# Optimization experiments

Measured on AMD Instinct MI355X. Metric: run time of the kernel, lower is better.

## Reference

```python
import jax, jax.numpy as jnp
import numpy as np

B, S, E_BERT = 64, 512, 768
H = 64        # GRU hidden per direction (hidden_dim=128 bidirectional)
T = 16        # num output tags
P = 32        # pos_num_tags = attention embed dim


def setup_inputs() -> dict:
    key = jax.random.key(0)
    ks = jax.random.split(key, 20)
    def n(k, shape, s=0.1):
        return jax.random.normal(k, shape, dtype=jnp.float32) * s
    return {
        "bert_embed": n(ks[0], (B, S, E_BERT), 1.0),
        "input2": n(ks[1], (B, S, P), 1.0),
        "targets": jax.random.randint(ks[2], (B, S), 0, T),
        # forward-direction GRU (torch layout: W_ih (3H,E), W_hh (3H,H))
        "Wih_f": n(ks[3], (3 * H, E_BERT)), "Whh_f": n(ks[4], (3 * H, H)),
        "bih_f": n(ks[5], (3 * H,)), "bhh_f": n(ks[6], (3 * H,)),
        # backward-direction GRU
        "Wih_b": n(ks[7], (3 * H, E_BERT)), "Whh_b": n(ks[8], (3 * H, H)),
        "bih_b": n(ks[9], (3 * H,)), "bhh_b": n(ks[10], (3 * H,)),
        # dense (no bias): (2H -> T)
        "Wdense": n(ks[11], (2 * H, T)),
        # single-head MultiheadAttention over pos features
        "in_proj_w": n(ks[12], (3 * P, P)), "in_proj_b": n(ks[13], (3 * P,)),
        "out_proj_w": n(ks[14], (P, P)), "out_proj_b": n(ks[15], (P,)),
        # fusion linear (no bias): (T+P -> T)
        "Wfuse": n(ks[16], (T + P, T)),
        # CRF params
        "crf_start": n(ks[17], (T,)), "crf_end": n(ks[18], (T,)),
        "crf_trans": n(ks[19], (T, T)),
    }


def _gru_dir(x, Wih, Whh, bih, bhh, reverse):
    # x: (B,S,E) -> outputs (B,S,H); torch GRU cell math.
    xp = jnp.einsum('bse,ge->bsg', x, Wih) + bih      # precompute input gates (B,S,3H)
    xp = jnp.swapaxes(xp, 0, 1)                        # (S,B,3H)
    h0 = jnp.zeros((x.shape[0], Whh.shape[1]), x.dtype)
    def step(h, xt):
        gh = h @ Whh.T + bhh
        xr, xz, xn = jnp.split(xt, 3, axis=-1)
        hr, hz, hn = jnp.split(gh, 3, axis=-1)
        r = jax.nn.sigmoid(xr + hr)
        z = jax.nn.sigmoid(xz + hz)
        nw = jnp.tanh(xn + r * hn)
        h = (1.0 - z) * nw + z * h
        return h, h
    _, ys = jax.lax.scan(step, h0, xp, reverse=reverse)
    return jnp.swapaxes(ys, 0, 1)                      # (B,S,H)


def _forward(bert_embed, input2, targets,
             Wih_f, Whh_f, bih_f, bhh_f,
             Wih_b, Whh_b, bih_b, bhh_b,
             Wdense, in_proj_w, in_proj_b, out_proj_w, out_proj_b,
             Wfuse, crf_start, crf_end, crf_trans):
    # Bi-GRU over frozen BERT embeddings
    fwd = _gru_dir(bert_embed, Wih_f, Whh_f, bih_f, bhh_f, False)
    bwd = _gru_dir(bert_embed, Wih_b, Whh_b, bih_b, bhh_b, True)
    lstm_out = jnp.concatenate([fwd, bwd], axis=-1)    # (B,S,2H)
    dense = lstm_out @ Wdense                          # (B,S,T)

    # single-head self-attention on POS features (torch MultiheadAttention)
    qkv = input2 @ in_proj_w.T + in_proj_b
    q, k, v = jnp.split(qkv, 3, axis=-1)
    scores = jnp.einsum('bqd,bkd->bqk', q, k) / jnp.sqrt(jnp.float32(P))
    attn = jnp.einsum('bqk,bkd->bqd', jax.nn.softmax(scores, axis=-1), v)
    attn = attn @ out_proj_w.T + out_proj_b            # (B,S,P)

    # fusion -> emissions
    emis = jnp.concatenate([dense, attn], axis=-1) @ Wfuse  # (B,S,T)

    # CRF NLL (torchcrf, full mask, reduction='mean')
    em_tags = jnp.take_along_axis(emis, targets[..., None], axis=2)[..., 0]  # (B,S)
    numerator = (crf_start[targets[:, 0]]
                 + em_tags.sum(axis=-1)
                 + crf_trans[targets[:, :-1], targets[:, 1:]].sum(axis=-1)
                 + crf_end[targets[:, -1]])

    def step(score, em_t):  # score (B,T), em_t (B,T)
        nxt = jax.nn.logsumexp(score[:, :, None] + crf_trans[None] + em_t[:, None, :], axis=1)
        return nxt, None
    score0 = crf_start[None] + emis[:, 0]
    scoreF, _ = jax.lax.scan(step, score0, jnp.swapaxes(emis[:, 1:], 0, 1))
    denominator = jax.nn.logsumexp(scoreF + crf_end[None], axis=1)

    return jnp.mean(denominator - numerator)  # -mean(log_likelihood)


def reference(bert_embed, input2, targets,
              Wih_f, Whh_f, bih_f, bhh_f,
              Wih_b, Whh_b, bih_b, bhh_b,
              Wdense, in_proj_w, in_proj_b, out_proj_w, out_proj_b,
              Wfuse, crf_start, crf_end, crf_trans):
    return _forward(bert_embed, input2, targets,
                    Wih_f, Whh_f, bih_f, bhh_f,
                    Wih_b, Whh_b, bih_b, bhh_b,
                    Wdense, in_proj_w, in_proj_b, out_proj_w, out_proj_b,
                    Wfuse, crf_start, crf_end, crf_trans)
```

## Files before the change

kernel.cpp:

```cpp
#include <hip/hip_runtime.h>

#define Bn 64
#define Sn 512
#define EB 768
#define Hn 64
#define G3 192
#define Tn 16
#define Pn 32

__device__ __forceinline__ float sigmoidf_(float x) { return 1.f / (1.f + __expf(-x)); }
__device__ __forceinline__ float tanhf_(float x) { return 1.f - 2.f / (__expf(2.f * x) + 1.f); }

__device__ __forceinline__ unsigned short f2bf(float x) {
  union { float f; unsigned u; } v; v.f = x;
  unsigned r = v.u + 0x7fff + ((v.u >> 16) & 1);
  return (unsigned short)(r >> 16);
}

typedef __attribute__((ext_vector_type(8))) short short8;
typedef __attribute__((ext_vector_type(4))) float f32x4;

__global__ __launch_bounds__(256) void mega_a(const float* __restrict__ A,
                                              const float* __restrict__ Wf,
                                              const float* __restrict__ Wb,
                                              const float* __restrict__ bf,
                                              const float* __restrict__ bb,
                                              float* __restrict__ C,
                                              const float* __restrict__ in2,
                                              const float* __restrict__ Wqkv,
                                              const float* __restrict__ bqkv,
                                              float* __restrict__ qb,
                                              float* __restrict__ kb,
                                              float* __restrict__ vb,
                                              const float* __restrict__ Wdense,
                                              const float* __restrict__ Wfuse,
                                              float* __restrict__ wcomb) {
  __shared__ __align__(16) char smem[20864];
  const int gblk = blockIdx.x;
  const int tid = threadIdx.x;
  if (gblk < 768) {
    unsigned short* As = (unsigned short*)smem;
    unsigned short* Bs = As + 128 * 40;
    const int g = gblk;
    const int xcd = g & 7;
    const int slot = g >> 3;
    const int lin = xcd * 96 + slot;
    const int m_tile = lin / 3;
    const int n_tile = lin % 3;
    const int n0 = n_tile * 128;
    const int m0 = m_tile * 128;
    const int wv = tid >> 6;
    const int lane = tid & 63;
    const int wm = (wv >> 1) * 64, wn = (wv & 1) * 64;
    const int fr = lane & 15, fq = lane >> 4;
    const int srow = tid >> 1;
    const int shalf = (tid & 1) * 16;
    const int bcol = n0 + srow;
    const float* Wrow = (bcol < G3) ? (Wf + (size_t)bcol * EB) : (Wb + (size_t)(bcol - G3) * EB);
    const float* Arow = A + (size_t)(m0 + srow) * EB;
    f32x4 acc[4][4];
#pragma unroll
    for (int i = 0; i < 4; ++i)
#pragma unroll
      for (int j = 0; j < 4; ++j) acc[i][j] = (f32x4){0.f, 0.f, 0.f, 0.f};
    for (int k0 = 0; k0 < EB; k0 += 32) {
      float4 a0 = *(const float4*)&Arow[k0 + shalf + 0];
      float4 a1 = *(const float4*)&Arow[k0 + shalf + 4];
      float4 a2 = *(const float4*)&Arow[k0 + shalf + 8];
      float4 a3 = *(const float4*)&Arow[k0 + shalf + 12];
      float4 b0 = *(const float4*)&Wrow[k0 + shalf + 0];
      float4 b1 = *(const float4*)&Wrow[k0 + shalf + 4];
      float4 b2 = *(const float4*)&Wrow[k0 + shalf + 8];
      float4 b3 = *(const float4*)&Wrow[k0 + shalf + 12];
      __syncthreads();
      short8 pa, pb;
      pa[0] = f2bf(a0.x); pa[1] = f2bf(a0.y); pa[2] = f2bf(a0.z); pa[3] = f2bf(a0.w);
      pa[4] = f2bf(a1.x); pa[5] = f2bf(a1.y); pa[6] = f2bf(a1.z); pa[7] = f2bf(a1.w);
      *(short8*)&As[srow * 40 + shalf] = pa;
      pa[0] = f2bf(a2.x); pa[1] = f2bf(a2.y); pa[2] = f2bf(a2.z); pa[3] = f2bf(a2.w);
      pa[4] = f2bf(a3.x); pa[5] = f2bf(a3.y); pa[6] = f2bf(a3.z); pa[7] = f2bf(a3.w);
      *(short8*)&As[srow * 40 + shalf + 8] = pa;
      pb[0] = f2bf(b0.x); pb[1] = f2bf(b0.y); pb[2] = f2bf(b0.z); pb[3] = f2bf(b0.w);
      pb[4] = f2bf(b1.x); pb[5] = f2bf(b1.y); pb[6] = f2bf(b1.z); pb[7] = f2bf(b1.w);
      *(short8*)&Bs[srow * 40 + shalf] = pb;
      pb[0] = f2bf(b2.x); pb[1] = f2bf(b2.y); pb[2] = f2bf(b2.z); pb[3] = f2bf(b2.w);
      pb[4] = f2bf(b3.x); pb[5] = f2bf(b3.y); pb[6] = f2bf(b3.z); pb[7] = f2bf(b3.w);
      *(short8*)&Bs[srow * 40 + shalf + 8] = pb;
      __syncthreads();
      short8 af[4], bfv[4];
#pragma unroll
      for (int i = 0; i < 4; ++i) af[i] = *(short8*)&As[(wm + i * 16 + fr) * 40 + fq * 8];
#pragma unroll
      for (int j = 0; j < 4; ++j) bfv[j] = *(short8*)&Bs[(wn + j * 16 + fr) * 40 + fq * 8];
#pragma unroll
      for (int i = 0; i < 4; ++i)
#pragma unroll
        for (int j = 0; j < 4; ++j)
          acc[i][j] = __builtin_amdgcn_mfma_f32_16x16x32_bf16(af[i], bfv[j], acc[i][j], 0, 0, 0);
    }
#pragma unroll
    for (int j = 0; j < 4; ++j) {
      int col = n0 + wn + j * 16 + fr;
      float bias = (col < G3) ? bf[col] : bb[col - G3];
#pragma unroll
      for (int i = 0; i < 4; ++i) {
        int rowb = m0 + wm + i * 16 + fq * 4;
#pragma unroll
        for (int rg = 0; rg < 4; ++rg)
          C[(size_t)(rowb + rg) * 384 + col] = acc[i][j][rg] + bias;
      }
    }
  } else if (gblk < 896) {
    float* Ws = (float*)smem;
    float* bs = Ws + 96 * 32;
    for (int i = tid; i < 96 * 32; i += 256) Ws[i] = Wqkv[i];
    if (tid < 96) bs[tid] = bqkv[tid];
    __syncthreads();
    const int idx = (gblk - 768) * 256 + tid;
    float x[32];
#pragma unroll
    for (int d4 = 0; d4 < 8; ++d4) {
      float4 v = *(const float4*)&in2[(size_t)idx * 32 + d4 * 4];
      x[d4 * 4 + 0] = v.x; x[d4 * 4 + 1] = v.y; x[d4 * 4 + 2] = v.z; x[d4 * 4 + 3] = v.w;
    }
    float* const dsts[3] = {qb, kb, vb};
#pragma unroll
    for (int p = 0; p < 3; ++p) {
      float a[32];
#pragma unroll
      for (int j = 0; j < 32; ++j) {
        float s = bs[p * 32 + j];
#pragma unroll
        for (int d = 0; d < 32; ++d) s += x[d] * Ws[(p * 32 + j) * 32 + d];
        a[j] = s;
      }
      float* dst = dsts[p];
#pragma unroll
      for (int j4 = 0; j4 < 8; ++j4) {
        float4 o = {a[j4 * 4 + 0], a[j4 * 4 + 1], a[j4 * 4 + 2], a[j4 * 4 + 3]};
        *(float4*)&dst[(size_t)idx * 32 + j4 * 4] = o;
      }
    }
  } else {
    int e = (gblk - 896) * 256 + tid;
    int i = e >> 4, j = e & 15;
    float a = 0.f;
#pragma unroll
    for (int c = 0; c < 16; ++c) a += Wdense[i * 16 + c] * Wfuse[c * 16 + j];
    wcomb[e] = a;
  }
}

__global__ __launch_bounds__(256, 1) void mega_b(const float* __restrict__ C,
                                                 const float* __restrict__ Whh_f,
                                                 const float* __restrict__ bhh_f,
                                                 const float* __restrict__ Whh_b,
                                                 const float* __restrict__ bhh_b,
                                                 float* __restrict__ out,
                                                 const float* __restrict__ qb,
                                                 const float* __restrict__ kb,
                                                 const float* __restrict__ vb,
                                                 float* __restrict__ part) {
  __shared__ __align__(16) char smem[33280];
  const int tid = threadIdx.x;
  if (blockIdx.x < 128) {
    float* xs = (float*)smem;
    float* hbuf = xs + 32 * 192;
    float* obuf = hbuf + 128;
    const int wg = blockIdx.x;
    const int rev = (wg >= Bn) ? 1 : 0;
    const int b = wg & (Bn - 1);
    const int w = tid >> 6;
    const int lane = tid & 63;
    const int r = lane >> 2;
    const int kc = lane & 3;
    const int row = 16 * w + r;
    const int k0 = 16 * kc;
    const float* Whh = rev ? Whh_b : Whh_f;
    const float* bhh = rev ? bhh_b : bhh_f;
    const int colBase = rev ? G3 : 0;
    const int dirOff = rev ? Hn : 0;
    float4 wv[3][4];
#pragma unroll
    for (int g = 0; g < 3; ++g)
#pragma unroll
      for (int q = 0; q < 4; ++q) {
        wv[g][q] = *(const float4*)&Whh[(size_t)(g * 64 + row) * 64 + k0 + 4 * q];
        asm volatile("" : "+v"(wv[g][q].x), "+v"(wv[g][q].y), "+v"(wv[g][q].z), "+v"(wv[g][q].w));
      }
    const float brr = bhh[row], bzz = bhh[64 + row], bnn = bhh[128 + row];
    if (tid < 64) { hbuf[tid] = 0.f; hbuf[64 + tid] = 0.f; }
    float h = 0.f;
    for (int c = 0; c < 16; ++c) {
      const int cstart = c * 32;
      if (c > 0) {
#pragma unroll
        for (int i = 0; i < 2; ++i) {
          int f = tid + 256 * i;
          int s = f >> 4;
          int c4 = (f & 15) << 2;
          int tp = cstart - 32 + s;
          int orow = rev ? (Sn - 1 - tp) : tp;
          *(float4*)&out[(size_t)(b * Sn + orow) * 128 + dirOff + c4] = *(const float4*)&obuf[s * 64 + c4];
        }
      }
      float4 st[6];
#pragma unroll
      for (int i = 0; i < 6; ++i) {
        int f = tid + 256 * i;
        int s = f / 48;
        int c4 = (f % 48) << 2;
        int t = cstart + s;
        int grow = rev ? (Sn - 1 - t) : t;
        st[i] = *(const float4*)&C[(size_t)(b * Sn + grow) * 384 + colBase + c4];
      }
#pragma unroll
      for (int i = 0; i < 6; ++i) {
        int f = tid + 256 * i;
        int s = f / 48;
        int c4 = (f % 48) << 2;
        *(float4*)&xs[s * 192 + c4] = st[i];
      }
      __syncthreads();
      float xr = xs[row], xz = xs[64 + row], xn = xs[128 + row];
      for (int s = 0; s < 32; ++s) {
        const int t = cstart + s;
        const int p = t & 1;
        float4 ha = *(const float4*)&hbuf[p * 64 + k0 + 0];
        float4 hb = *(const float4*)&hbuf[p * 64 + k0 + 4];
        float4 hc = *(const float4*)&hbuf[p * 64 + k0 + 8];
        float4 hd = *(const float4*)&hbuf[p * 64 + k0 + 12];
        float nxr = 0.f, nxz = 0.f, nxn = 0.f;
        if (s + 1 < 32) {
          const float* xq = &xs[(s + 1) * 192];
          nxr = xq[row]; nxz = xq[64 + row]; nxn = xq[128 + row];
        }
        float dr, dz, dn;
        {
          float4 wa, wbv, wc, wd;
          wa = wv[0][0]; wbv = wv[0][1]; wc = wv[0][2]; wd = wv[0][3];
          dr = (wa.x * ha.x + wa.y * ha.y + wa.z * ha.z + wa.w * ha.w)
             + (wbv.x * hb.x + wbv.y * hb.y + wbv.z * hb.z + wbv.w * hb.w)
             + (wc.x * hc.x + wc.y * hc.y + wc.z * hc.z + wc.w * hc.w)
             + (wd.x * hd.x + wd.y * hd.y + wd.z * hd.z + wd.w * hd.w);
          wa = wv[1][0]; wbv = wv[1][1]; wc = wv[1][2]; wd = wv[1][3];
          dz = (wa.x * ha.x + wa.y * ha.y + wa.z * ha.z + wa.w * ha.w)
             + (wbv.x * hb.x + wbv.y * hb.y + wbv.z * hb.z + wbv.w * hb.w)
             + (wc.x * hc.x + wc.y * hc.y + wc.z * hc.z + wc.w * hc.w)
             + (wd.x * hd.x + wd.y * hd.y + wd.z * hd.z + wd.w * hd.w);
          wa = wv[2][0]; wbv = wv[2][1]; wc = wv[2][2]; wd = wv[2][3];
          dn = (wa.x * ha.x + wa.y * ha.y + wa.z * ha.z + wa.w * ha.w)
             + (wbv.x * hb.x + wbv.y * hb.y + wbv.z * hb.z + wbv.w * hb.w)
             + (wc.x * hc.x + wc.y * hc.y + wc.z * hc.z + wc.w * hc.w)
             + (wd.x * hd.x + wd.y * hd.y + wd.z * hd.z + wd.w * hd.w);
        }
        dr += __shfl_xor(dr, 1); dr += __shfl_xor(dr, 2);
        dz += __shfl_xor(dz, 1); dz += __shfl_xor(dz, 2);
        dn += __shfl_xor(dn, 1); dn += __shfl_xor(dn, 2);
        float rg = sigmoidf_(xr + brr + dr);
        float zg = sigmoidf_(xz + bzz + dz);
        float ng = tanhf_(xn + rg * (bnn + dn));
        h = (1.f - zg) * ng + zg * h;
        if (kc == 0) {
          hbuf[(p ^ 1) * 64 + row] = h;
          obuf[s * 64 + row] = h;
        }
        __syncthreads();
        xr = nxr; xz = nxz; xn = nxn;
      }
    }
#pragma unroll
    for (int i = 0; i < 2; ++i) {
      int f = tid + 256 * i;
      int s = f >> 4;
      int c4 = (f & 15) << 2;
      int tp = Sn - 32 + s;
      int orow = rev ? (Sn - 1 - tp) : tp;
      *(float4*)&out[(size_t)(b * Sn + orow) * 128 + dirOff + c4] = *(const float4*)&obuf[s * 64 + c4];
    }
  } else {
    float* Ks = (float*)smem;
    float* Vs = Ks + 128 * 32;
    const int blk = blockIdx.x - 128;
    const int b = blk >> 3;
    const int qhalf = (blk >> 2) & 1;
    const int split = blk & 3;
    const int k0 = split * 128;
#pragma unroll
    for (int i = 0; i < 4; ++i) {
      int f = tid + 256 * i;
      int row = f >> 3, col = (f & 7) * 4;
      *(float4*)&Ks[row * 32 + col] = *(const float4*)&kb[(size_t)(b * Sn + k0 + row) * 32 + col];
      *(float4*)&Vs[row * 32 + col] = *(const float4*)&vb[(size_t)(b * Sn + k0 + row) * 32 + col];
    }
    const int q = b * Sn + qhalf * 256 + tid;
    float qv[32];
#pragma unroll
    for (int d4 = 0; d4 < 8; ++d4) {
      float4 v = *(const float4*)&qb[(size_t)q * 32 + d4 * 4];
      qv[d4 * 4 + 0] = v.x; qv[d4 * 4 + 1] = v.y; qv[d4 * 4 + 2] = v.z; qv[d4 * 4 + 3] = v.w;
    }
    __syncthreads();
    const float scale = 0.17677669529663687f;
    float m = -1e30f, lsum = 0.f;
    float acc[32] = {};
    for (int kk = 0; kk < 128; ++kk) {
      const float4* kr = (const float4*)&Ks[kk * 32];
      float s = 0.f;
#pragma unroll
      for (int d4 = 0; d4 < 8; ++d4) {
        float4 kv = kr[d4];
        s += qv[d4 * 4 + 0] * kv.x + qv[d4 * 4 + 1] * kv.y + qv[d4 * 4 + 2] * kv.z + qv[d4 * 4 + 3] * kv.w;
      }
      s *= scale;
      float mn = fmaxf(m, s);
      float e1 = __expf(m - mn);
      float p = __expf(s - mn);
      lsum = lsum * e1 + p;
      const float4* vr = (const float4*)&Vs[kk * 32];
#pragma unroll
      for (int d4 = 0; d4 < 8; ++d4) {
        float4 vv = vr[d4];
        acc[d4 * 4 + 0] = acc[d4 * 4 + 0] * e1 + p * vv.x;
        acc[d4 * 4 + 1] = acc[d4 * 4 + 1] * e1 + p * vv.y;
        acc[d4 * 4 + 2] = acc[d4 * 4 + 2] * e1 + p * vv.z;
        acc[d4 * 4 + 3] = acc[d4 * 4 + 3] * e1 + p * vv.w;
      }
      m = mn;
    }
    float* rec = part + ((size_t)q * 4 + split) * 36;
#pragma unroll
    for (int d4 = 0; d4 < 8; ++d4) {
      float4 o = {acc[d4 * 4 + 0], acc[d4 * 4 + 1], acc[d4 * 4 + 2], acc[d4 * 4 + 3]};
      *(float4*)&rec[d4 * 4] = o;
    }
    rec[32] = m;
    rec[33] = lsum;
  }
}

__global__ __launch_bounds__(256) void attn_combine(const float* __restrict__ part,
                                                    const float* __restrict__ Wout,
                                                    const float* __restrict__ bout,
                                                    float* __restrict__ attn) {
  __shared__ float Ws[32 * 32];
  __shared__ float bs[32];
  const int tid = threadIdx.x;
  for (int i = tid; i < 1024; i += 256) Ws[i] = Wout[i];
  if (tid < 32) bs[tid] = bout[tid];
  __syncthreads();
  const int q = blockIdx.x * 256 + tid;
  const float* rec = part + (size_t)q * 4 * 36;
  float m0 = rec[32], m1 = rec[36 + 32], m2 = rec[72 + 32], m3 = rec[108 + 32];
  float M = fmaxf(fmaxf(m0, m1), fmaxf(m2, m3));
  float w0 = __expf(m0 - M), w1 = __expf(m1 - M), w2 = __expf(m2 - M), w3 = __expf(m3 - M);
  float L = rec[33] * w0 + rec[36 + 33] * w1 + rec[72 + 33] * w2 + rec[108 + 33] * w3;
  float inv = 1.f / L;
  float a[32];
#pragma unroll
  for (int d4 = 0; d4 < 8; ++d4) {
    float4 p0 = *(const float4*)&rec[d4 * 4];
    float4 p1 = *(const float4*)&rec[36 + d4 * 4];
    float4 p2 = *(const float4*)&rec[72 + d4 * 4];
    float4 p3 = *(const float4*)&rec[108 + d4 * 4];
    a[d4 * 4 + 0] = (p0.x * w0 + p1.x * w1 + p2.x * w2 + p3.x * w3) * inv;
    a[d4 * 4 + 1] = (p0.y * w0 + p1.y * w1 + p2.y * w2 + p3.y * w3) * inv;
    a[d4 * 4 + 2] = (p0.z * w0 + p1.z * w1 + p2.z * w2 + p3.z * w3) * inv;
    a[d4 * 4 + 3] = (p0.w * w0 + p1.w * w1 + p2.w * w2 + p3.w * w3) * inv;
  }
#pragma unroll
  for (int j = 0; j < 32; ++j) {
    float o = bs[j];
#pragma unroll
    for (int d = 0; d < 32; ++d) o += a[d] * Ws[j * 32 + d];
    attn[(size_t)q * 32 + j] = o;
  }
}

__global__ __launch_bounds__(256) void emis_kernel(const float* __restrict__ lstm,
                                                   const float* __restrict__ attn,
                                                   const float* __restrict__ wcomb,
                                                   const float* __restrict__ Wfuse,
                                                   float* __restrict__ emis) {
  __shared__ float Wc[128 * 16];
  __shared__ float Wf2[32 * 16];
  const int tid = threadIdx.x;
  for (int i = tid; i < 2048; i += 256) Wc[i] = wcomb[i];
  for (int i = tid; i < 512; i += 256) Wf2[i] = Wfuse[16 * 16 + i];
  __syncthreads();
  const int idx = blockIdx.x * 256 + tid;
  float acc[16] = {};
  for (int i = 0; i < 128; i += 4) {
    float4 lv = *(const float4*)&lstm[(size_t)idx * 128 + i];
    float ll[4] = {lv.x, lv.y, lv.z, lv.w};
#pragma unroll
    for (int u = 0; u < 4; ++u)
#pragma unroll
      for (int j = 0; j < 16; ++j) acc[j] += ll[u] * Wc[(i + u) * 16 + j];
  }
  for (int d = 0; d < 32; d += 4) {
    float4 av = *(const float4*)&attn[(size_t)idx * 32 + d];
    float aa[4] = {av.x, av.y, av.z, av.w};
#pragma unroll
    for (int u = 0; u < 4; ++u)
#pragma unroll
      for (int j = 0; j < 16; ++j) acc[j] += aa[u] * Wf2[(d + u) * 16 + j];
  }
#pragma unroll
  for (int j = 0; j < 16; j += 4) {
    float4 o = {acc[j], acc[j + 1], acc[j + 2], acc[j + 3]};
    *(float4*)&emis[(size_t)idx * 16 + j] = o;
  }
}

__global__ __launch_bounds__(64) void mega_e(const float* __restrict__ emis,
                                             const int* __restrict__ tgt,
                                             const float* __restrict__ cstart,
                                             const float* __restrict__ cend,
                                             const float* __restrict__ ctrans,
                                             float* __restrict__ numer,
                                             float* __restrict__ denom) {
  if (blockIdx.x < 64) {
    const int b = blockIdx.x, l = threadIdx.x;
    float ssum = 0.f;
    for (int t = l; t < Sn; t += 64) {
      int tg = tgt[b * Sn + t];
      ssum += emis[(size_t)(b * Sn + t) * Tn + tg];
      if (t + 1 < Sn) {
        int tg2 = tgt[b * Sn + t + 1];
        ssum += ctrans[tg * Tn + tg2];
      }
    }
    if (l == 0) ssum += cstart[tgt[b * Sn]] + cend[tgt[b * Sn + Sn - 1]];
    for (int off = 32; off > 0; off >>= 1) ssum += __shfl_down(ssum, off);
    if (l == 0) numer[b] = ssum;
  } else {
    const int b = blockIdx.x - 64;
    const int lane = threadIdx.x;
    const int g = lane >> 4;
    const int j = lane & 15;
    const int i0 = 4 * g;
    float tr0 = ctrans[(i0 + 0) * Tn + j];
    float tr1 = ctrans[(i0 + 1) * Tn + j];
    float tr2 = ctrans[(i0 + 2) * Tn + j];
    float tr3 = ctrans[(i0 + 3) * Tn + j];
    float s = cstart[j] + emis[(size_t)(b * Sn) * Tn + j];
    float em = emis[(size_t)(b * Sn + 1) * Tn + j];
    for (int t = 1; t < Sn; ++t) {
      float s0 = __shfl(s, i0 + 0);
      float s1 = __shfl(s, i0 + 1);
      float s2 = __shfl(s, i0 + 2);
      float s3 = __shfl(s, i0 + 3);
      float v0 = s0 + tr0, v1 = s1 + tr1, v2 = s2 + tr2, v3 = s3 + tr3;
      float m = fmaxf(fmaxf(v0, v1), fmaxf(v2, v3));
      m = fmaxf(m, __shfl_xor(m, 16));
      m = fmaxf(m, __shfl_xor(m, 32));
      float e = __expf(v0 - m) + __expf(v1 - m) + __expf(v2 - m) + __expf(v3 - m);
      e += __shfl_xor(e, 16);
      e += __shfl_xor(e, 32);
      float em_cur = em;
      if (t + 1 < Sn) em = emis[(size_t)(b * Sn + t + 1) * Tn + j];
      s = em_cur + m + __logf(e);
    }
    float f = s + cend[j];
    float m = f;
    m = fmaxf(m, __shfl_xor(m, 1));
    m = fmaxf(m, __shfl_xor(m, 2));
    m = fmaxf(m, __shfl_xor(m, 4));
    m = fmaxf(m, __shfl_xor(m, 8));
    float e = __expf(f - m);
    e += __shfl_xor(e, 1);
    e += __shfl_xor(e, 2);
    e += __shfl_xor(e, 4);
    e += __shfl_xor(e, 8);
    if (lane == 0) denom[b] = m + __logf(e);
  }
}

__global__ __launch_bounds__(64) void final_kernel(const float* __restrict__ numer,
                                                   const float* __restrict__ denom,
                                                   float* __restrict__ out) {
  const int l = threadIdx.x;
  float d = denom[l] - numer[l];
  for (int off = 32; off > 0; off >>= 1) d += __shfl_down(d, off);
  if (l == 0) out[0] = d * (1.f / 64.f);
}

extern "C" void kernel_launch(void* const* d_in, const int* in_sizes, int n_in,
                              void* d_out, int out_size, void* d_ws, size_t ws_size,
                              hipStream_t stream) {
  (void)in_sizes; (void)n_in; (void)out_size; (void)ws_size;
  const float* bert = (const float*)d_in[0];
  const float* in2 = (const float*)d_in[1];
  const int* tgt = (const int*)d_in[2];
  const float* Wih_f = (const float*)d_in[3];
  const float* Whh_f = (const float*)d_in[4];
  const float* bih_f = (const float*)d_in[5];
  const float* bhh_f = (const float*)d_in[6];
  const float* Wih_b = (const float*)d_in[7];
  const float* Whh_b = (const float*)d_in[8];
  const float* bih_b = (const float*)d_in[9];
  const float* bhh_b = (const float*)d_in[10];
  const float* Wdense = (const float*)d_in[11];
  const float* in_proj_w = (const float*)d_in[12];
  const float* in_proj_b = (const float*)d_in[13];
  const float* out_proj_w = (const float*)d_in[14];
  const float* out_proj_b = (const float*)d_in[15];
  const float* Wfuse = (const float*)d_in[16];
  const float* cstart = (const float*)d_in[17];
  const float* cend = (const float*)d_in[18];
  const float* ctrans = (const float*)d_in[19];

  float* ws = (float*)d_ws;
  float* C = ws;
  float* lstm = C + (size_t)Bn * Sn * 384;
  float* qb = lstm + (size_t)Bn * Sn * 2 * Hn;
  float* kb = qb + (size_t)Bn * Sn * Pn;
  float* vb = kb + (size_t)Bn * Sn * Pn;
  float* attn = vb + (size_t)Bn * Sn * Pn;
  float* emis = attn + (size_t)Bn * Sn * Pn;
  float* wcomb = emis + (size_t)Bn * Sn * Tn;
  float* numer = wcomb + 128 * 16;
  float* denom = numer + Bn;
  float* part = denom + Bn;

  mega_a<<<904, 256, 0, stream>>>(bert, Wih_f, Wih_b, bih_f, bih_b, C,
                                  in2, in_proj_w, in_proj_b, qb, kb, vb,
                                  Wdense, Wfuse, wcomb);
  mega_b<<<640, 256, 0, stream>>>(C, Whh_f, bhh_f, Whh_b, bhh_b, lstm,
                                  qb, kb, vb, part);
  attn_combine<<<Bn * Sn / 256, 256, 0, stream>>>(part, out_proj_w, out_proj_b, attn);
  emis_kernel<<<Bn * Sn / 256, 256, 0, stream>>>(lstm, attn, wcomb, Wfuse, emis);
  mega_e<<<128, 64, 0, stream>>>(emis, tgt, cstart, cend, ctrans, numer, denom);
  final_kernel<<<1, 64, 0, stream>>>(numer, denom, (float*)d_out);
}
```

Before: 621.1 us.

## Pre-convert GEMM operands to bf16 and use direct global-to-LDS loads; fuse attn combine with emission

Adds a separate pass that converts bert embeddings and input weights to bf16 in workspace. The input-projection GEMM then streams them into LDS with global_load_lds instead of loading fp32, converting in registers and storing to LDS. The attention-combine and emission kernels are merged so the attention output stays in registers and is never written to or reread from global memory. The conversion pass reads the full fp32 tensor and writes a bf16 copy, which adds traffic and a launch. The GEMM also drops LDS padding, which may cause bank conflicts, and its loop has no double buffering.

Measured after the change: 704.2 us. 1.13x slower.

```diff
diff --git a/kernel.cpp b/kernel.cpp
--- a/kernel.cpp
+++ b/kernel.cpp
@@ -20,9 +20,34 @@
 typedef __attribute__((ext_vector_type(8))) short short8;
 typedef __attribute__((ext_vector_type(4))) float f32x4;
 
-__global__ __launch_bounds__(256) void mega_a(const float* __restrict__ A,
-                                              const float* __restrict__ Wf,
-                                              const float* __restrict__ Wb,
+__device__ __forceinline__ void gload_lds16(const unsigned short* g, unsigned short* l) {
+  __builtin_amdgcn_global_load_lds((const __attribute__((address_space(1))) unsigned int*)g,
+                                   (__attribute__((address_space(3))) unsigned int*)l, 16, 0, 0);
+}
+
+__global__ __launch_bounds__(256) void convert_kernel(const float* __restrict__ bert,
+                                                      const float* __restrict__ Wf,
+                                                      const float* __restrict__ Wb,
+                                                      unsigned short* __restrict__ Abf,
+                                                      unsigned short* __restrict__ Wbf) {
+  const int blk = blockIdx.x;
+  const float* src;
+  unsigned short* dst;
+  size_t base;
+  if (blk < 12288) { src = bert; dst = Abf; base = (size_t)blk * 2048; }
+  else if (blk < 12360) { src = Wf; dst = Wbf; base = (size_t)(blk - 12288) * 2048; }
+  else { src = Wb; dst = Wbf + 147456; base = (size_t)(blk - 12360) * 2048; }
+  size_t e = base + (size_t)threadIdx.x * 8;
+  float4 v0 = *(const float4*)&src[e];
+  float4 v1 = *(const float4*)&src[e + 4];
+  short8 o;
+  o[0] = f2bf(v0.x); o[1] = f2bf(v0.y); o[2] = f2bf(v0.z); o[3] = f2bf(v0.w);
+  o[4] = f2bf(v1.x); o[5] = f2bf(v1.y); o[6] = f2bf(v1.z); o[7] = f2bf(v1.w);
+  *(short8*)&dst[e] = o;
+}
+
+__global__ __launch_bounds__(256) void mega_a(const unsigned short* __restrict__ Abf,
+                                              const unsigned short* __restrict__ Wbf,
                                               const float* __restrict__ bf,
                                               const float* __restrict__ bb,
                                               float* __restrict__ C,
@@ -35,15 +60,14 @@
                                               const float* __restrict__ Wdense,
                                               const float* __restrict__ Wfuse,
                                               float* __restrict__ wcomb) {
-  __shared__ __align__(16) char smem[20864];
+  __shared__ __align__(16) char smem[16384];
   const int gblk = blockIdx.x;
   const int tid = threadIdx.x;
   if (gblk < 768) {
     unsigned short* As = (unsigned short*)smem;
-    unsigned short* Bs = As + 128 * 40;
-    const int g = gblk;
-    const int xcd = g & 7;
-    const int slot = g >> 3;
+    unsigned short* Bs = As + 128 * 32;
+    const int xcd = gblk & 7;
+    const int slot = gblk >> 3;
     const int lin = xcd * 96 + slot;
     const int m_tile = lin / 3;
     const int n_tile = lin % 3;
@@ -53,50 +77,38 @@
     const int lane = tid & 63;
     const int wm = (wv >> 1) * 64, wn = (wv & 1) * 64;
     const int fr = lane & 15, fq = lane >> 4;
-    const int srow = tid >> 1;
-    const int shalf = (tid & 1) * 16;
-    const int bcol = n0 + srow;
-    const float* Wrow = (bcol < G3) ? (Wf + (size_t)bcol * EB) : (Wb + (size_t)(bcol - G3) * EB);
-    const float* Arow = A + (size_t)(m0 + srow) * EB;
+    const int c0 = (wv * 2 + 0) * 64 + lane;
+    const int c1 = (wv * 2 + 1) * 64 + lane;
+    const unsigned short* Asrc0 = Abf + (size_t)(m0 + (c0 >> 2)) * EB + (c0 & 3) * 8;
+    const unsigned short* Asrc1 = Abf + (size_t)(m0 + (c1 >> 2)) * EB + (c1 & 3) * 8;
+    const unsigned short* Bsrc0 = Wbf + (size_t)(n0 + (c0 >> 2)) * EB + (c0 & 3) * 8;
+    const unsigned short* Bsrc1 = Wbf + (size_t)(n0 + (c1 >> 2)) * EB + (c1 & 3) * 8;
+    unsigned short* Adst0 = As + (wv * 2 + 0) * 64 * 8;
+    unsigned short* Adst1 = As + (wv * 2 + 1) * 64 * 8;
+    unsigned short* Bdst0 = Bs + (wv * 2 + 0) * 64 * 8;
+    unsigned short* Bdst1 = Bs + (wv * 2 + 1) * 64 * 8;
     f32x4 acc[4][4];
 #pragma unroll
     for (int i = 0; i < 4; ++i)
 #pragma unroll
       for (int j = 0; j < 4; ++j) acc[i][j] = (f32x4){0.f, 0.f, 0.f, 0.f};
     for (int k0 = 0; k0 < EB; k0 += 32) {
-      float4 a0 = *(const float4*)&Arow[k0 + shalf + 0];
-      float4 a1 = *(const float4*)&Arow[k0 + shalf + 4];
-      float4 a2 = *(const float4*)&Arow[k0 + shalf + 8];
-      float4 a3 = *(const float4*)&Arow[k0 + shalf + 12];
-      float4 b0 = *(const float4*)&Wrow[k0 + shalf + 0];
-      float4 b1 = *(const float4*)&Wrow[k0 + shalf + 4];
-      float4 b2 = *(const float4*)&Wrow[k0 + shalf + 8];
-      float4 b3 = *(const float4*)&Wrow[k0 + shalf + 12];
-      __syncthreads();
-      short8 pa, pb;
-      pa[0] = f2bf(a0.x); pa[1] = f2bf(a0.y); pa[2] = f2bf(a0.z); pa[3] = f2bf(a0.w);
-      pa[4] = f2bf(a1.x); pa[5] = f2bf(a1.y); pa[6] = f2bf(a1.z); pa[7] = f2bf(a1.w);
-      *(short8*)&As[srow * 40 + shalf] = pa;
-      pa[0] = f2bf(a2.x); pa[1] = f2bf(a2.y); pa[2] = f2bf(a2.z); pa[3] = f2bf(a2.w);
-      pa[4] = f2bf(a3.x); pa[5] = f2bf(a3.y); pa[6] = f2bf(a3.z); pa[7] = f2bf(a3.w);
-      *(short8*)&As[srow * 40 + shalf + 8] = pa;
-      pb[0] = f2bf(b0.x); pb[1] = f2bf(b0.y); pb[2] = f2bf(b0.z); pb[3] = f2bf(b0.w);
-      pb[4] = f2bf(b1.x); pb[5] = f2bf(b1.y); pb[6] = f2bf(b1.z); pb[7] = f2bf(b1.w);
-      *(short8*)&Bs[srow * 40 + shalf] = pb;
-      pb[0] = f2bf(b2.x); pb[1] = f2bf(b2.y); pb[2] = f2bf(b2.z); pb[3] = f2bf(b2.w);
-      pb[4] = f2bf(b3.x); pb[5] = f2bf(b3.y); pb[6] = f2bf(b3.z); pb[7] = f2bf(b3.w);
-      *(short8*)&Bs[srow * 40 + shalf + 8] = pb;
+      gload_lds16(Asrc0 + k0, Adst0);
+      gload_lds16(Asrc1 + k0, Adst1);
+      gload_lds16(Bsrc0 + k0, Bdst0);
+      gload_lds16(Bsrc1 + k0, Bdst1);
       __syncthreads();
       short8 af[4], bfv[4];
 #pragma unroll
-      for (int i = 0; i < 4; ++i) af[i] = *(short8*)&As[(wm + i * 16 + fr) * 40 + fq * 8];
-#pragma unroll
-      for (int j = 0; j < 4; ++j) bfv[j] = *(short8*)&Bs[(wn + j * 16 + fr) * 40 + fq * 8];
+      for (int i = 0; i < 4; ++i) af[i] = *(short8*)&As[(wm + i * 16 + fr) * 32 + fq * 8];
+#pragma unroll
+      for (int j = 0; j < 4; ++j) bfv[j] = *(short8*)&Bs[(wn + j * 16 + fr) * 32 + fq * 8];
 #pragma unroll
       for (int i = 0; i < 4; ++i)
 #pragma unroll
         for (int j = 0; j < 4; ++j)
           acc[i][j] = __builtin_amdgcn_mfma_f32_16x16x32_bf16(af[i], bfv[j], acc[i][j], 0, 0, 0);
+      __syncthreads();
     }
 #pragma unroll
     for (int j = 0; j < 4; ++j) {
@@ -339,15 +351,22 @@
   }
 }
 
-__global__ __launch_bounds__(256) void attn_combine(const float* __restrict__ part,
-                                                    const float* __restrict__ Wout,
-                                                    const float* __restrict__ bout,
-                                                    float* __restrict__ attn) {
+__global__ __launch_bounds__(256) void comb_emis(const float* __restrict__ part,
+                                                 const float* __restrict__ Wout,
+                                                 const float* __restrict__ bout,
+                                                 const float* __restrict__ lstm,
+                                                 const float* __restrict__ wcomb,
+                                                 const float* __restrict__ Wfuse,
+                                                 float* __restrict__ emis) {
   __shared__ float Ws[32 * 32];
   __shared__ float bs[32];
+  __shared__ float Wc[128 * 16];
+  __shared__ float Wf2[32 * 16];
   const int tid = threadIdx.x;
   for (int i = tid; i < 1024; i += 256) Ws[i] = Wout[i];
   if (tid < 32) bs[tid] = bout[tid];
+  for (int i = tid; i < 2048; i += 256) Wc[i] = wcomb[i];
+  for (int i = tid; i < 512; i += 256) Wf2[i] = Wfuse[16 * 16 + i];
   __syncthreads();
   const int q = blockIdx.x * 256 + tid;
   const float* rec = part + (size_t)q * 4 * 36;
@@ -368,48 +387,31 @@
     a[d4 * 4 + 2] = (p0.z * w0 + p1.z * w1 + p2.z * w2 + p3.z * w3) * inv;
     a[d4 * 4 + 3] = (p0.w * w0 + p1.w * w1 + p2.w * w2 + p3.w * w3) * inv;
   }
+  float o[32];
 #pragma unroll
   for (int j = 0; j < 32; ++j) {
-    float o = bs[j];
-#pragma unroll
-    for (int d = 0; d < 32; ++d) o += a[d] * Ws[j * 32 + d];
-    attn[(size_t)q * 32 + j] = o;
-  }
-}
-
-__global__ __launch_bounds__(256) void emis_kernel(const float* __restrict__ lstm,
-                                                   const float* __restrict__ attn,
-                                                   const float* __restrict__ wcomb,
-                                                   const float* __restrict__ Wfuse,
-                                                   float* __restrict__ emis) {
-  __shared__ float Wc[128 * 16];
-  __shared__ float Wf2[32 * 16];
-  const int tid = threadIdx.x;
-  for (int i = tid; i < 2048; i += 256) Wc[i] = wcomb[i];
-  for (int i = tid; i < 512; i += 256) Wf2[i] = Wfuse[16 * 16 + i];
-  __syncthreads();
-  const int idx = blockIdx.x * 256 + tid;
+    float s = bs[j];
+#pragma unroll
+    for (int d = 0; d < 32; ++d) s += a[d] * Ws[j * 32 + d];
+    o[j] = s;
+  }
   float acc[16] = {};
   for (int i = 0; i < 128; i += 4) {
-    float4 lv = *(const float4*)&lstm[(size_t)idx * 128 + i];
+    float4 lv = *(const float4*)&lstm[(size_t)q * 128 + i];
     float ll[4] = {lv.x, lv.y, lv.z, lv.w};
 #pragma unroll
     for (int u = 0; u < 4; ++u)
 #pragma unroll
       for (int j = 0; j < 16; ++j) acc[j] += ll[u] * Wc[(i + u) * 16 + j];
   }
-  for (int d = 0; d < 32; d += 4) {
-    float4 av = *(const float4*)&attn[(size_t)idx * 32 + d];
-    float aa[4] = {av.x, av.y, av.z, av.w};
-#pragma unroll
-    for (int u = 0; u < 4; ++u)
-#pragma unroll
-      for (int j = 0; j < 16; ++j) acc[j] += aa[u] * Wf2[(d + u) * 16 + j];
-  }
+#pragma unroll
+  for (int d = 0; d < 32; ++d)
+#pragma unroll
+    for (int j = 0; j < 16; ++j) acc[j] += o[d] * Wf2[d * 16 + j];
 #pragma unroll
   for (int j = 0; j < 16; j += 4) {
-    float4 o = {acc[j], acc[j + 1], acc[j + 2], acc[j + 3]};
-    *(float4*)&emis[(size_t)idx * 16 + j] = o;
+    float4 ov = {acc[j], acc[j + 1], acc[j + 2], acc[j + 3]};
+    *(float4*)&emis[(size_t)q * 16 + j] = ov;
   }
 }
 
@@ -513,24 +515,27 @@
 
   float* ws = (float*)d_ws;
   float* C = ws;
-  float* lstm = C + (size_t)Bn * Sn * 384;
-  float* qb = lstm + (size_t)Bn * Sn * 2 * Hn;
-  float* kb = qb + (size_t)Bn * Sn * Pn;
-  float* vb = kb + (size_t)Bn * Sn * Pn;
-  float* attn = vb + (size_t)Bn * Sn * Pn;
-  float* emis = attn + (size_t)Bn * Sn * Pn;
-  float* wcomb = emis + (size_t)Bn * Sn * Tn;
-  float* numer = wcomb + 128 * 16;
-  float* denom = numer + Bn;
-  float* part = denom + Bn;
-
-  mega_a<<<904, 256, 0, stream>>>(bert, Wih_f, Wih_b, bih_f, bih_b, C,
+  float* lstm = C + (size_t)12582912;
+  float* qb = lstm + (size_t)4194304;
+  float* kb = qb + (size_t)1048576;
+  float* vb = kb + (size_t)1048576;
+  float* wcomb = vb + (size_t)1048576;
+  float* numer = wcomb + 2048;
+  float* denom = numer + 64;
+  float* region = denom + 64;
+  unsigned short* Abf = (unsigned short*)region;
+  float* emis = region;
+  float* part = emis + (size_t)524288;
+  unsigned short* Wbf = (unsigned short*)(region + (size_t)12582912);
+
+  convert_kernel<<<12432, 256, 0, stream>>>(bert, Wih_f, Wih_b, Abf, Wbf);
+  mega_a<<<904, 256, 0, stream>>>(Abf, Wbf, bih_f, bih_b, C,
                                   in2, in_proj_w, in_proj_b, qb, kb, vb,
                                   Wdense, Wfuse, wcomb);
   mega_b<<<640, 256, 0, stream>>>(C, Whh_f, bhh_f, Whh_b, bhh_b, lstm,
                                   qb, kb, vb, part);
-  attn_combine<<<Bn * Sn / 256, 256, 0, stream>>>(part, out_proj_w, out_proj_b, attn);
-  emis_kernel<<<Bn * Sn / 256, 256, 0, stream>>>(lstm, attn, wcomb, Wfuse, emis);
+  comb_emis<<<Bn * Sn / 256, 256, 0, stream>>>(part, out_proj_w, out_proj_b,
+                                               lstm, wcomb, Wfuse, emis);
   mega_e<<<128, 64, 0, stream>>>(emis, tgt, cstart, cend, ctrans, numer, denom);
   final_kernel<<<1, 64, 0, stream>>>(numer, denom, (float*)d_out);
 }
```

## Fuse attention combine into emission kernel, batch CRF chains, cheaper bf16 packing

Applied to the files above, without the earlier changes.

Merges the attention-combine and emission kernels so the attention output stays in registers and never goes through global memory, removing one launch and one intermediate buffer. The CRF forward recursion now processes four batch rows per wavefront, interleaving independent chains to hide shuffle and exp latency, which cuts the denominator blocks from 64 to 16. The GEMM's float-to-bf16 conversion switches from round-to-nearest-even to truncation via a byte permute, so fewer ALU ops are spent packing but rounding accuracy is slightly lower.

New measurement: 865.8 us. 39.4% more time.

```diff
diff --git a/kernel.cpp b/kernel.cpp
--- a/kernel.cpp
+++ b/kernel.cpp
@@ -11,10 +11,8 @@
 __device__ __forceinline__ float sigmoidf_(float x) { return 1.f / (1.f + __expf(-x)); }
 __device__ __forceinline__ float tanhf_(float x) { return 1.f - 2.f / (__expf(2.f * x) + 1.f); }
 
-__device__ __forceinline__ unsigned short f2bf(float x) {
-  union { float f; unsigned u; } v; v.f = x;
-  unsigned r = v.u + 0x7fff + ((v.u >> 16) & 1);
-  return (unsigned short)(r >> 16);
+__device__ __forceinline__ unsigned pkbf(float a, float b) {
+  return __builtin_amdgcn_perm(__float_as_uint(b), __float_as_uint(a), 0x07060302u);
 }
 
 typedef __attribute__((ext_vector_type(8))) short short8;
@@ -41,9 +39,8 @@
   if (gblk < 768) {
     unsigned short* As = (unsigned short*)smem;
     unsigned short* Bs = As + 128 * 40;
-    const int g = gblk;
-    const int xcd = g & 7;
-    const int slot = g >> 3;
+    const int xcd = gblk & 7;
+    const int slot = gblk >> 3;
     const int lin = xcd * 96 + slot;
     const int m_tile = lin / 3;
     const int n_tile = lin % 3;
@@ -73,19 +70,19 @@
       float4 b2 = *(const float4*)&Wrow[k0 + shalf + 8];
       float4 b3 = *(const float4*)&Wrow[k0 + shalf + 12];
       __syncthreads();
-      short8 pa, pb;
-      pa[0] = f2bf(a0.x); pa[1] = f2bf(a0.y); pa[2] = f2bf(a0.z); pa[3] = f2bf(a0.w);
-      pa[4] = f2bf(a1.x); pa[5] = f2bf(a1.y); pa[6] = f2bf(a1.z); pa[7] = f2bf(a1.w);
-      *(short8*)&As[srow * 40 + shalf] = pa;
-      pa[0] = f2bf(a2.x); pa[1] = f2bf(a2.y); pa[2] = f2bf(a2.z); pa[3] = f2bf(a2.w);
-      pa[4] = f2bf(a3.x); pa[5] = f2bf(a3.y); pa[6] = f2bf(a3.z); pa[7] = f2bf(a3.w);
-      *(short8*)&As[srow * 40 + shalf + 8] = pa;
-      pb[0] = f2bf(b0.x); pb[1] = f2bf(b0.y); pb[2] = f2bf(b0.z); pb[3] = f2bf(b0.w);
-      pb[4] = f2bf(b1.x); pb[5] = f2bf(b1.y); pb[6] = f2bf(b1.z); pb[7] = f2bf(b1.w);
-      *(short8*)&Bs[srow * 40 + shalf] = pb;
-      pb[0] = f2bf(b2.x); pb[1] = f2bf(b2.y); pb[2] = f2bf(b2.z); pb[3] = f2bf(b2.w);
-      pb[4] = f2bf(b3.x); pb[5] = f2bf(b3.y); pb[6] = f2bf(b3.z); pb[7] = f2bf(b3.w);
-      *(short8*)&Bs[srow * 40 + shalf + 8] = pb;
+      uint4 w;
+      w.x = pkbf(a0.x, a0.y); w.y = pkbf(a0.z, a0.w);
+      w.z = pkbf(a1.x, a1.y); w.w = pkbf(a1.z, a1.w);
+      *(uint4*)&As[srow * 40 + shalf] = w;
+      w.x = pkbf(a2.x, a2.y); w.y = pkbf(a2.z, a2.w);
+      w.z = pkbf(a3.x, a3.y); w.w = pkbf(a3.z, a3.w);
+      *(uint4*)&As[srow * 40 + shalf + 8] = w;
+      w.x = pkbf(b0.x, b0.y); w.y = pkbf(b0.z, b0.w);
+      w.z = pkbf(b1.x, b1.y); w.w = pkbf(b1.z, b1.w);
+      *(uint4*)&Bs[srow * 40 + shalf] = w;
+      w.x = pkbf(b2.x, b2.y); w.y = pkbf(b2.z, b2.w);
+      w.z = pkbf(b3.x, b3.y); w.w = pkbf(b3.z, b3.w);
+      *(uint4*)&Bs[srow * 40 + shalf + 8] = w;
       __syncthreads();
       short8 af[4], bfv[4];
 #pragma unroll
@@ -339,15 +336,22 @@
   }
 }
 
-__global__ __launch_bounds__(256) void attn_combine(const float* __restrict__ part,
-                                                    const float* __restrict__ Wout,
-                                                    const float* __restrict__ bout,
-                                                    float* __restrict__ attn) {
+__global__ __launch_bounds__(256) void comb_emis(const float* __restrict__ part,
+                                                 const float* __restrict__ Wout,
+                                                 const float* __restrict__ bout,
+                                                 const float* __restrict__ lstm,
+                                                 const float* __restrict__ wcomb,
+                                                 const float* __restrict__ Wfuse,
+                                                 float* __restrict__ emis) {
   __shared__ float Ws[32 * 32];
   __shared__ float bs[32];
+  __shared__ float Wc[128 * 16];
+  __shared__ float Wf2[32 * 16];
   const int tid = threadIdx.x;
   for (int i = tid; i < 1024; i += 256) Ws[i] = Wout[i];
   if (tid < 32) bs[tid] = bout[tid];
+  for (int i = tid; i < 2048; i += 256) Wc[i] = wcomb[i];
+  for (int i = tid; i < 512; i += 256) Wf2[i] = Wfuse[16 * 16 + i];
   __syncthreads();
   const int q = blockIdx.x * 256 + tid;
   const float* rec = part + (size_t)q * 4 * 36;
@@ -368,48 +372,31 @@
     a[d4 * 4 + 2] = (p0.z * w0 + p1.z * w1 + p2.z * w2 + p3.z * w3) * inv;
     a[d4 * 4 + 3] = (p0.w * w0 + p1.w * w1 + p2.w * w2 + p3.w * w3) * inv;
   }
+  float o[32];
 #pragma unroll
   for (int j = 0; j < 32; ++j) {
-    float o = bs[j];
-#pragma unroll
-    for (int d = 0; d < 32; ++d) o += a[d] * Ws[j * 32 + d];
-    attn[(size_t)q * 32 + j] = o;
-  }
-}
-
-__global__ __launch_bounds__(256) void emis_kernel(const float* __restrict__ lstm,
-                                                   const float* __restrict__ attn,
-                                                   const float* __restrict__ wcomb,
-                                                   const float* __restrict__ Wfuse,
-                                                   float* __restrict__ emis) {
-  __shared__ float Wc[128 * 16];
-  __shared__ float Wf2[32 * 16];
-  const int tid = threadIdx.x;
-  for (int i = tid; i < 2048; i += 256) Wc[i] = wcomb[i];
-  for (int i = tid; i < 512; i += 256) Wf2[i] = Wfuse[16 * 16 + i];
-  __syncthreads();
-  const int idx = blockIdx.x * 256 + tid;
+    float s = bs[j];
+#pragma unroll
+    for (int d = 0; d < 32; ++d) s += a[d] * Ws[j * 32 + d];
+    o[j] = s;
+  }
   float acc[16] = {};
   for (int i = 0; i < 128; i += 4) {
-    float4 lv = *(const float4*)&lstm[(size_t)idx * 128 + i];
+    float4 lv = *(const float4*)&lstm[(size_t)q * 128 + i];
     float ll[4] = {lv.x, lv.y, lv.z, lv.w};
 #pragma unroll
     for (int u = 0; u < 4; ++u)
 #pragma unroll
       for (int j = 0; j < 16; ++j) acc[j] += ll[u] * Wc[(i + u) * 16 + j];
   }
-  for (int d = 0; d < 32; d += 4) {
-    float4 av = *(const float4*)&attn[(size_t)idx * 32 + d];
-    float aa[4] = {av.x, av.y, av.z, av.w};
-#pragma unroll
-    for (int u = 0; u < 4; ++u)
-#pragma unroll
-      for (int j = 0; j < 16; ++j) acc[j] += aa[u] * Wf2[(d + u) * 16 + j];
-  }
+#pragma unroll
+  for (int d = 0; d < 32; ++d)
+#pragma unroll
+    for (int j = 0; j < 16; ++j) acc[j] += o[d] * Wf2[d * 16 + j];
 #pragma unroll
   for (int j = 0; j < 16; j += 4) {
-    float4 o = {acc[j], acc[j + 1], acc[j + 2], acc[j + 3]};
-    *(float4*)&emis[(size_t)idx * 16 + j] = o;
+    float4 ov = {acc[j], acc[j + 1], acc[j + 2], acc[j + 3]};
+    *(float4*)&emis[(size_t)q * 16 + j] = ov;
   }
 }
 
@@ -435,7 +422,7 @@
     for (int off = 32; off > 0; off >>= 1) ssum += __shfl_down(ssum, off);
     if (l == 0) numer[b] = ssum;
   } else {
-    const int b = blockIdx.x - 64;
+    const int b0 = (blockIdx.x - 64) * 4;
     const int lane = threadIdx.x;
     const int g = lane >> 4;
     const int j = lane & 15;
@@ -444,36 +431,48 @@
     float tr1 = ctrans[(i0 + 1) * Tn + j];
     float tr2 = ctrans[(i0 + 2) * Tn + j];
     float tr3 = ctrans[(i0 + 3) * Tn + j];
-    float s = cstart[j] + emis[(size_t)(b * Sn) * Tn + j];
-    float em = emis[(size_t)(b * Sn + 1) * Tn + j];
+    const float cs = cstart[j];
+    float sB[4], emB[4];
+#pragma unroll
+    for (int u = 0; u < 4; ++u) {
+      sB[u] = cs + emis[(size_t)((b0 + u) * Sn) * Tn + j];
+      emB[u] = emis[(size_t)((b0 + u) * Sn + 1) * Tn + j];
+    }
     for (int t = 1; t < Sn; ++t) {
-      float s0 = __shfl(s, i0 + 0);
-      float s1 = __shfl(s, i0 + 1);
-      float s2 = __shfl(s, i0 + 2);
-      float s3 = __shfl(s, i0 + 3);
-      float v0 = s0 + tr0, v1 = s1 + tr1, v2 = s2 + tr2, v3 = s3 + tr3;
-      float m = fmaxf(fmaxf(v0, v1), fmaxf(v2, v3));
-      m = fmaxf(m, __shfl_xor(m, 16));
-      m = fmaxf(m, __shfl_xor(m, 32));
-      float e = __expf(v0 - m) + __expf(v1 - m) + __expf(v2 - m) + __expf(v3 - m);
-      e += __shfl_xor(e, 16);
-      e += __shfl_xor(e, 32);
-      float em_cur = em;
-      if (t + 1 < Sn) em = emis[(size_t)(b * Sn + t + 1) * Tn + j];
-      s = em_cur + m + __logf(e);
-    }
-    float f = s + cend[j];
-    float m = f;
-    m = fmaxf(m, __shfl_xor(m, 1));
-    m = fmaxf(m, __shfl_xor(m, 2));
-    m = fmaxf(m, __shfl_xor(m, 4));
-    m = fmaxf(m, __shfl_xor(m, 8));
-    float e = __expf(f - m);
-    e += __shfl_xor(e, 1);
-    e += __shfl_xor(e, 2);
-    e += __shfl_xor(e, 4);
-    e += __shfl_xor(e, 8);
-    if (lane == 0) denom[b] = m + __logf(e);
+#pragma unroll
+      for (int u = 0; u < 4; ++u) {
+        float s0 = __shfl(sB[u], i0 + 0);
+        float s1 = __shfl(sB[u], i0 + 1);
+        float s2 = __shfl(sB[u], i0 + 2);
+        float s3 = __shfl(sB[u], i0 + 3);
+        float v0 = s0 + tr0, v1 = s1 + tr1, v2 = s2 + tr2, v3 = s3 + tr3;
+        float m = fmaxf(fmaxf(v0, v1), fmaxf(v2, v3));
+        m = fmaxf(m, __shfl_xor(m, 16));
+        m = fmaxf(m, __shfl_xor(m, 32));
+        float e = __expf(v0 - m) + __expf(v1 - m) + __expf(v2 - m) + __expf(v3 - m);
+        e += __shfl_xor(e, 16);
+        e += __shfl_xor(e, 32);
+        float em_cur = emB[u];
+        if (t + 1 < Sn) emB[u] = emis[(size_t)((b0 + u) * Sn + t + 1) * Tn + j];
+        sB[u] = em_cur + m + __logf(e);
+      }
+    }
+    const float ce = cend[j];
+#pragma unroll
+    for (int u = 0; u < 4; ++u) {
+      float f = sB[u] + ce;
+      float m = f;
+      m = fmaxf(m, __shfl_xor(m, 1));
+      m = fmaxf(m, __shfl_xor(m, 2));
+      m = fmaxf(m, __shfl_xor(m, 4));
+      m = fmaxf(m, __shfl_xor(m, 8));
+      float e = __expf(f - m);
+      e += __shfl_xor(e, 1);
+      e += __shfl_xor(e, 2);
+      e += __shfl_xor(e, 4);
+      e += __shfl_xor(e, 8);
+      if (lane == 0) denom[b0 + u] = m + __logf(e);
+    }
   }
 }
 
@@ -517,10 +516,9 @@
   float* qb = lstm + (size_t)Bn * Sn * 2 * Hn;
   float* kb = qb + (size_t)Bn * Sn * Pn;
   float* vb = kb + (size_t)Bn * Sn * Pn;
-  float* attn = vb + (size_t)Bn * Sn * Pn;
-  float* emis = attn + (size_t)Bn * Sn * Pn;
+  float* emis = vb + (size_t)Bn * Sn * Pn;
   float* wcomb = emis + (size_t)Bn * Sn * Tn;
-  float* numer = wcomb + 128 * 16;
+  float* numer = wcomb + 2048;
   float* denom = numer + Bn;
   float* part = denom + Bn;
 
@@ -529,8 +527,8 @@
                                   Wdense, Wfuse, wcomb);
   mega_b<<<640, 256, 0, stream>>>(C, Whh_f, bhh_f, Whh_b, bhh_b, lstm,
                                   qb, kb, vb, part);
-  attn_combine<<<Bn * Sn / 256, 256, 0, stream>>>(part, out_proj_w, out_proj_b, attn);
-  emis_kernel<<<Bn * Sn / 256, 256, 0, stream>>>(lstm, attn, wcomb, Wfuse, emis);
-  mega_e<<<128, 64, 0, stream>>>(emis, tgt, cstart, cend, ctrans, numer, denom);
+  comb_emis<<<Bn * Sn / 256, 256, 0, stream>>>(part, out_proj_w, out_proj_b,
+                                               lstm, wcomb, Wfuse, emis);
+  mega_e<<<80, 64, 0, stream>>>(emis, tgt, cstart, cend, ctrans, numer, denom);
   final_kernel<<<1, 64, 0, stream>>>(numer, denom, (float*)d_out);
 }
```

## Parallelize CRF forward recursion via chunked log-semiring matrix products

Applied to the files above, without the earlier changes.

The serial 511-step CRF partition recursion is split into 8 chunks per batch. A new scan kernel computes each chunk's 16x16 log-semiring transfer matrix in parallel, and mega_e then combines the 8 matrices with the initial vector. This replaces a long per-batch serial chain with shorter chains spread across more blocks. The cost is one extra kernel launch, 16x more logsumexp work per step, a barrier on every step, and an extra workspace buffer.

New measurement: 545.3 us. -12.2%, faster.

```diff
diff --git a/kernel.cpp b/kernel.cpp
--- a/kernel.cpp
+++ b/kernel.cpp
@@ -41,9 +41,8 @@
   if (gblk < 768) {
     unsigned short* As = (unsigned short*)smem;
     unsigned short* Bs = As + 128 * 40;
-    const int g = gblk;
-    const int xcd = g & 7;
-    const int slot = g >> 3;
+    const int xcd = gblk & 7;
+    const int slot = gblk >> 3;
     const int lin = xcd * 96 + slot;
     const int m_tile = lin / 3;
     const int n_tile = lin % 3;
@@ -413,11 +412,57 @@
   }
 }
 
+__global__ __launch_bounds__(256) void scan_kernel(const float* __restrict__ emis,
+                                                   const float* __restrict__ ctrans,
+                                                   float* __restrict__ scanbuf) {
+  __shared__ __align__(16) float P[16 * 20];
+  const int blk = blockIdx.x;
+  const int b = blk >> 3;
+  const int g = blk & 7;
+  const int tid = threadIdx.x;
+  const int i = tid >> 4;
+  const int j = tid & 15;
+  const int t0 = 1 + 64 * g;
+  const int t1 = (64 + 64 * g < 511) ? (64 + 64 * g) : 511;
+  float trk[16];
+#pragma unroll
+  for (int k = 0; k < 16; ++k) trk[k] = ctrans[k * 16 + j];
+  P[i * 20 + j] = ctrans[i * 16 + j] + emis[((size_t)(b * Sn + t0)) * Tn + j];
+  float em_next = emis[((size_t)(b * Sn + t0 + 1)) * Tn + j];
+  __syncthreads();
+  float out = 0.f;
+  for (int t = t0 + 1; t <= t1; ++t) {
+    float4 r0 = *(const float4*)&P[i * 20 + 0];
+    float4 r1 = *(const float4*)&P[i * 20 + 4];
+    float4 r2 = *(const float4*)&P[i * 20 + 8];
+    float4 r3 = *(const float4*)&P[i * 20 + 12];
+    float em_t = em_next;
+    if (t + 1 <= t1) em_next = emis[((size_t)(b * Sn + t + 1)) * Tn + j];
+    float wk[16];
+    wk[0] = r0.x + trk[0]; wk[1] = r0.y + trk[1]; wk[2] = r0.z + trk[2]; wk[3] = r0.w + trk[3];
+    wk[4] = r1.x + trk[4]; wk[5] = r1.y + trk[5]; wk[6] = r1.z + trk[6]; wk[7] = r1.w + trk[7];
+    wk[8] = r2.x + trk[8]; wk[9] = r2.y + trk[9]; wk[10] = r2.z + trk[10]; wk[11] = r2.w + trk[11];
+    wk[12] = r3.x + trk[12]; wk[13] = r3.y + trk[13]; wk[14] = r3.z + trk[14]; wk[15] = r3.w + trk[15];
+    float m = wk[0];
+#pragma unroll
+    for (int k = 1; k < 16; ++k) m = fmaxf(m, wk[k]);
+    float e = 0.f;
+#pragma unroll
+    for (int k = 0; k < 16; ++k) e += __expf(wk[k] - m);
+    out = m + __logf(e) + em_t;
+    __syncthreads();
+    P[i * 20 + j] = out;
+    __syncthreads();
+  }
+  scanbuf[((size_t)blk) * 256 + i * 16 + j] = P[i * 20 + j];
+}
+
 __global__ __launch_bounds__(64) void mega_e(const float* __restrict__ emis,
                                              const int* __restrict__ tgt,
                                              const float* __restrict__ cstart,
                                              const float* __restrict__ cend,
                                              const float* __restrict__ ctrans,
+                                             const float* __restrict__ scanbuf,
                                              float* __restrict__ numer,
                                              float* __restrict__ denom) {
   if (blockIdx.x < 64) {
@@ -435,34 +480,35 @@
     for (int off = 32; off > 0; off >>= 1) ssum += __shfl_down(ssum, off);
     if (l == 0) numer[b] = ssum;
   } else {
+    __shared__ __align__(16) float vbuf[16];
     const int b = blockIdx.x - 64;
     const int lane = threadIdx.x;
-    const int g = lane >> 4;
     const int j = lane & 15;
-    const int i0 = 4 * g;
-    float tr0 = ctrans[(i0 + 0) * Tn + j];
-    float tr1 = ctrans[(i0 + 1) * Tn + j];
-    float tr2 = ctrans[(i0 + 2) * Tn + j];
-    float tr3 = ctrans[(i0 + 3) * Tn + j];
-    float s = cstart[j] + emis[(size_t)(b * Sn) * Tn + j];
-    float em = emis[(size_t)(b * Sn + 1) * Tn + j];
-    for (int t = 1; t < Sn; ++t) {
-      float s0 = __shfl(s, i0 + 0);
-      float s1 = __shfl(s, i0 + 1);
-      float s2 = __shfl(s, i0 + 2);
-      float s3 = __shfl(s, i0 + 3);
-      float v0 = s0 + tr0, v1 = s1 + tr1, v2 = s2 + tr2, v3 = s3 + tr3;
-      float m = fmaxf(fmaxf(v0, v1), fmaxf(v2, v3));
-      m = fmaxf(m, __shfl_xor(m, 16));
-      m = fmaxf(m, __shfl_xor(m, 32));
-      float e = __expf(v0 - m) + __expf(v1 - m) + __expf(v2 - m) + __expf(v3 - m);
-      e += __shfl_xor(e, 16);
-      e += __shfl_xor(e, 32);
-      float em_cur = em;
-      if (t + 1 < Sn) em = emis[(size_t)(b * Sn + t + 1) * Tn + j];
-      s = em_cur + m + __logf(e);
-    }
-    float f = s + cend[j];
+    float v = cstart[j] + emis[(size_t)(b * Sn) * Tn + j];
+    if (lane < 16) vbuf[j] = v;
+    for (int g = 0; g < 8; ++g) {
+      float4 v0 = *(const float4*)&vbuf[0];
+      float4 v1 = *(const float4*)&vbuf[4];
+      float4 v2 = *(const float4*)&vbuf[8];
+      float4 v3 = *(const float4*)&vbuf[12];
+      const float* P = scanbuf + ((size_t)(b * 8 + g)) * 256;
+      float wk[16];
+#pragma unroll
+      for (int k = 0; k < 16; ++k) wk[k] = P[k * 16 + j];
+      wk[0] += v0.x; wk[1] += v0.y; wk[2] += v0.z; wk[3] += v0.w;
+      wk[4] += v1.x; wk[5] += v1.y; wk[6] += v1.z; wk[7] += v1.w;
+      wk[8] += v2.x; wk[9] += v2.y; wk[10] += v2.z; wk[11] += v2.w;
+      wk[12] += v3.x; wk[13] += v3.y; wk[14] += v3.z; wk[15] += v3.w;
+      float m = wk[0];
+#pragma unroll
+      for (int k = 1; k < 16; ++k) m = fmaxf(m, wk[k]);
+      float e = 0.f;
+#pragma unroll
+      for (int k = 0; k < 16; ++k) e += __expf(wk[k] - m);
+      float nv = m + __logf(e);
+      if (lane < 16) vbuf[j] = nv;
+    }
+    float f = vbuf[j] + cend[j];
     float m = f;
     m = fmaxf(m, __shfl_xor(m, 1));
     m = fmaxf(m, __shfl_xor(m, 2));
@@ -520,9 +566,10 @@
   float* attn = vb + (size_t)Bn * Sn * Pn;
   float* emis = attn + (size_t)Bn * Sn * Pn;
   float* wcomb = emis + (size_t)Bn * Sn * Tn;
-  float* numer = wcomb + 128 * 16;
+  float* numer = wcomb + 2048;
   float* denom = numer + Bn;
   float* part = denom + Bn;
+  float* scanbuf = part + (size_t)32768 * 4 * 36;
 
   mega_a<<<904, 256, 0, stream>>>(bert, Wih_f, Wih_b, bih_f, bih_b, C,
                                   in2, in_proj_w, in_proj_b, qb, kb, vb,
@@ -531,6 +578,7 @@
                                   qb, kb, vb, part);
   attn_combine<<<Bn * Sn / 256, 256, 0, stream>>>(part, out_proj_w, out_proj_b, attn);
   emis_kernel<<<Bn * Sn / 256, 256, 0, stream>>>(lstm, attn, wcomb, Wfuse, emis);
-  mega_e<<<128, 64, 0, stream>>>(emis, tgt, cstart, cend, ctrans, numer, denom);
+  scan_kernel<<<Bn * 8, 256, 0, stream>>>(emis, ctrans, scanbuf);
+  mega_e<<<128, 64, 0, stream>>>(emis, tgt, cstart, cend, ctrans, scanbuf, numer, denom);
   final_kernel<<<1, 64, 0, stream>>>(numer, denom, (float*)d_out);
 }
```
